# Kernel optimization log

Measured on AMD Instinct MI355X. Metric: run time of the kernel, lower is better.

## Reference

```python
import jax, jax.numpy as jnp
import numpy as np


def setup_inputs() -> dict:
    key = jax.random.key(0)
    ks = jax.random.split(key, 7)
    C, IC, H, W, B = 512, 256, 64, 64, 8
    N = H * W
    return {
        "x": jax.random.normal(ks[0], (B, C, H, W), dtype=jnp.float32),
        "w_phi": jax.random.normal(ks[1], (IC, C), dtype=jnp.float32) * 0.02,
        "w_theta": jax.random.normal(ks[2], (IC, C), dtype=jnp.float32) * 0.02,
        "w_g": jax.random.normal(ks[3], (IC, C), dtype=jnp.float32) * 0.02,
        "w_mask": jax.random.normal(ks[4], (C, IC), dtype=jnp.float32) * 0.02,
        "pos_embedding": jax.random.normal(ks[5], (1, N, N), dtype=jnp.float32),
        "pos_embedding_decoder": jax.random.normal(ks[6], (1, IC, H, W), dtype=jnp.float32),
    }


def reference(x, w_phi, w_theta, w_g, w_mask, pos_embedding, pos_embedding_decoder):
    b, c, h, w = x.shape
    n = h * w
    xf = x.reshape(b, c, n)  # [b, c, n]
    # 1x1 convs as channel matmuls
    phi = jnp.einsum('oc,bcn->bon', w_phi, xf)      # [b, ic, n]
    theta = jnp.einsum('oc,bcn->bon', w_theta, xf)  # [b, ic, n]
    g = jnp.einsum('oc,bcn->bon', w_g, xf) + pos_embedding_decoder.reshape(1, -1, n)
    g = jnp.swapaxes(g, 1, 2)  # [b, n, ic]
    # attention logits: theta^T @ phi -> [b, n_theta, n_phi], plus learned pos bias
    attn = jnp.einsum('bci,bcj->bij', theta, phi) + pos_embedding
    # NOTE: original softmax is over dim=1 (the theta/query axis), non-standard
    attn = jax.nn.softmax(attn, axis=1)
    y = jnp.einsum('bij,bjc->bic', attn, g)  # [b, n, ic]
    y = jnp.swapaxes(y, 1, 2).reshape(b, -1, n)  # [b, ic, n]
    mask = jnp.einsum('oc,bcn->bon', w_mask, y).reshape(b, c, h, w)
    return mask + x
```

## Files before the change

kernel.cpp:

```cpp
#include <hip/hip_runtime.h>

typedef short bf8 __attribute__((ext_vector_type(8)));
typedef float f32x4 __attribute__((ext_vector_type(4)));
typedef unsigned short us4 __attribute__((ext_vector_type(4)));
typedef unsigned short us8 __attribute__((ext_vector_type(8)));

#define DEVI __device__ __forceinline__

constexpr int NB = 8, NC = 512, NIC = 256, NS = 4096;

constexpr size_t OFF_XT  = 0;
constexpr size_t OFF_RS  = 0;
constexpr size_t OFF_TP  = 33554432;
constexpr size_t OFF_POS = 67108864;
constexpr size_t OFF_G   = 100663296;
constexpr size_t OFF_G2  = 117440512;
constexpr size_t OFF_Y   = 134217728;
constexpr size_t OFF_WTP = 150994944;
constexpr size_t OFF_WG  = 151519232;
constexpr size_t OFF_WM  = 151781376;

DEVI unsigned short f2bf(float f){
  unsigned u = __float_as_uint(f);
  u += 0x7fffu + ((u >> 16) & 1u);
  return (unsigned short)(u >> 16);
}
DEVI float bf2f(unsigned short b){ return __uint_as_float(((unsigned)b) << 16); }

DEVI void gld16(const void* g, void* l){
  __builtin_amdgcn_global_load_lds((const __attribute__((address_space(1))) unsigned int*)g,
                                   (__attribute__((address_space(3))) unsigned int*)l, 16, 0, 0);
}

DEVI void stageT(unsigned short* dst, const unsigned short* src, int ld, int wid, int lane){
  int rl = lane >> 3;
  int ce = ((lane & 7) << 3) ^ (rl << 3);
#pragma unroll
  for (int it = 0; it < 4; ++it){
    int q = wid + it * 4;
    gld16(src + (size_t)(q * 8 + rl) * ld + ce, dst + q * 512);
  }
}

DEVI void zero44(f32x4 (&a)[4][4]){
  f32x4 z = {0.f, 0.f, 0.f, 0.f};
#pragma unroll
  for (int i = 0; i < 4; ++i)
#pragma unroll
    for (int j = 0; j < 4; ++j) a[i][j] = z;
}

template<int NK64>
DEVI void gemm128v(const unsigned short* Ag, int lda, const unsigned short* Bg, int ldb,
                   unsigned short (&As)[2][8192], unsigned short (&Bs)[2][8192],
                   f32x4 (&acc)[4][4], int wid, int lane)
{
  const int wr = wid >> 1, wc = wid & 1;
  stageT(As[0], Ag, lda, wid, lane);
  stageT(Bs[0], Bg, ldb, wid, lane);
  __syncthreads();
  for (int kt = 0; kt < NK64; ++kt){
    int cur = kt & 1;
    if (kt + 1 < NK64){
      stageT(As[cur ^ 1], Ag + (kt + 1) * 64, lda, wid, lane);
      stageT(Bs[cur ^ 1], Bg + (kt + 1) * 64, ldb, wid, lane);
    }
    bf8 a[2][4], b[2][4];
#pragma unroll
    for (int ks = 0; ks < 2; ++ks){
      int cb = ks * 64 + ((lane >> 4) << 4);
#pragma unroll
      for (int f = 0; f < 4; ++f){
        int rA = wr * 64 + f * 16 + (lane & 15);
        a[ks][f] = *(const bf8*)((char*)As[cur] + rA * 128 + (cb ^ ((rA & 7) << 4)));
        int rB = wc * 64 + f * 16 + (lane & 15);
        b[ks][f] = *(const bf8*)((char*)Bs[cur] + rB * 128 + (cb ^ ((rB & 7) << 4)));
      }
    }
    __builtin_amdgcn_s_setprio(1);
#pragma unroll
    for (int ks = 0; ks < 2; ++ks)
#pragma unroll
      for (int i = 0; i < 4; ++i)
#pragma unroll
        for (int j = 0; j < 4; ++j)
          acc[i][j] = __builtin_amdgcn_mfma_f32_16x16x32_bf16(a[ks][i], b[ks][j], acc[i][j], 0, 0, 0);
    __builtin_amdgcn_s_setprio(0);
    __syncthreads();
  }
}


__global__ void k_prep(const float* wphi, const float* wtheta, const float* wgf, const float* wmf,
                       unsigned short* wtp, unsigned short* wgb, unsigned short* wmb){
  int idx = (blockIdx.x * 256 + threadIdx.x) * 4;
  const float* src; unsigned short* dst;
  if (idx < 131072)      { src = wphi + idx;            dst = wtp + idx; }
  else if (idx < 262144) { src = wtheta + (idx - 131072); dst = wtp + idx; }
  else if (idx < 393216) { src = wgf + (idx - 262144);  dst = wgb + (idx - 262144); }
  else                   { src = wmf + (idx - 393216);  dst = wmb + (idx - 393216); }
  f32x4 v = *(const f32x4*)src;
  us4 o;
#pragma unroll
  for (int r = 0; r < 4; ++r) o[r] = f2bf(v[r]);
  *(us4*)dst = o;
}

__global__ void k_pos(const float* pos, unsigned short* posb){
  size_t base = ((size_t)blockIdx.x * 256 + threadIdx.x) * 8;
  f32x4 v0 = *(const f32x4*)&pos[base];
  f32x4 v1 = *(const f32x4*)&pos[base + 4];
  us8 o;
#pragma unroll
  for (int r = 0; r < 4; ++r){ o[r] = f2bf(v0[r]); o[r + 4] = f2bf(v1[r]); }
  *(us8*)&posb[base] = o;
}

__global__ void k_xt(const float* x, unsigned short* xT){
  int b = blockIdx.z, ct = blockIdx.y, nt = blockIdx.x;
  __shared__ float t[64][65];
  int tid = threadIdx.x;
  int c0 = ct * 64, n0 = nt * 64;
  const float* xp = x + (size_t)b * NC * NS;
#pragma unroll
  for (int it = 0; it < 16; ++it){
    int idx = it * 256 + tid; int r = idx >> 6, cc = idx & 63;
    t[r][cc] = xp[(size_t)(c0 + r) * NS + n0 + cc];
  }
  __syncthreads();
  unsigned short* xo = xT + (size_t)b * NS * NC;
#pragma unroll
  for (int it = 0; it < 16; ++it){
    int idx = it * 256 + tid; int r = idx >> 6, cc = idx & 63;
    xo[(size_t)(n0 + r) * NC + c0 + cc] = f2bf(t[cc][r]);
  }
}


__global__ __launch_bounds__(256, 2) void k_tp(const unsigned short* wtp, const unsigned short* xT,
                                               unsigned short* tp){
  int b = blockIdx.z, ot = blockIdx.y, nt = blockIdx.x;
  int tid = threadIdx.x, wid = tid >> 6, lane = tid & 63, wr = wid >> 1, wc = wid & 1;
  __shared__ unsigned short As[2][8192], Bs[2][8192];
  f32x4 acc[4][4]; zero44(acc);
  gemm128v<8>(wtp + (size_t)(ot * 128) * 512, 512,
              xT + ((size_t)b * NS + nt * 128) * 512, 512, As, Bs, acc, wid, lane);
  unsigned short* out = tp + (size_t)b * NS * 512;
#pragma unroll
  for (int fr = 0; fr < 4; ++fr)
#pragma unroll
    for (int fc = 0; fc < 4; ++fc){
      int o0 = ot * 128 + wr * 64 + fr * 16 + ((lane >> 4) << 2);
      int n  = nt * 128 + wc * 64 + fc * 16 + (lane & 15);
      us4 v;
#pragma unroll
      for (int r = 0; r < 4; ++r) v[r] = f2bf(acc[fr][fc][r]);
      *(us4*)&out[(size_t)n * 512 + o0] = v;
    }
}

__global__ __launch_bounds__(256, 2) void k_g(const unsigned short* xT, const unsigned short* wgb,
                                              const float* pdec, unsigned short* gb){
  int b = blockIdx.z, ot = blockIdx.y, nt = blockIdx.x;
  int tid = threadIdx.x, wid = tid >> 6, lane = tid & 63, wr = wid >> 1, wc = wid & 1;
  __shared__ unsigned short As[2][8192], Bs[2][8192];
  f32x4 acc[4][4]; zero44(acc);
  gemm128v<8>(xT + ((size_t)b * NS + nt * 128) * 512, 512,
              wgb + (size_t)(ot * 128) * 512, 512, As, Bs, acc, wid, lane);
#pragma unroll
  for (int fr = 0; fr < 4; ++fr)
#pragma unroll
    for (int fc = 0; fc < 4; ++fc){
      int n0 = nt * 128 + wr * 64 + fr * 16 + ((lane >> 4) << 2);
      int o  = ot * 128 + wc * 64 + fc * 16 + (lane & 15);
      f32x4 pd = *(const f32x4*)&pdec[(size_t)o * NS + n0];
      us4 v;
#pragma unroll
      for (int r = 0; r < 4; ++r) v[r] = f2bf(acc[fr][fc][r] + pd[r]);
      *(us4*)&gb[((size_t)b * NIC + o) * NS + n0] = v;
    }
}

__global__ __launch_bounds__(256, 2) void k_stats(const unsigned short* __restrict__ tp,
                                                  const unsigned short* __restrict__ posb,
                                                  float* __restrict__ rs){
  int bid = blockIdx.x;
  int b = bid & 7, jb0 = (bid >> 3) * 64;
  int tid = threadIdx.x, wid = tid >> 6, lane = tid & 63;
  int p = wid >> 1, q = wid & 1, h = lane >> 4, l15 = lane & 15;
  __shared__ unsigned short Ath[4][8192];
  __shared__ float red[64];
  const unsigned short* tpb = tp + (size_t)b * NS * 512;

  bf8 bphi[8][2];
#pragma unroll
  for (int kb = 0; kb < 8; ++kb)
#pragma unroll
    for (int frj = 0; frj < 2; ++frj)
      bphi[kb][frj] = *(const bf8*)&tpb[(size_t)(jb0 + p * 32 + frj * 16 + l15) * 512
                                        + kb * 32 + h * 8];

  float sacc[2][4];
#pragma unroll
  for (int a = 0; a < 2; ++a)
#pragma unroll
    for (int r = 0; r < 4; ++r) sacc[a][r] = 0.f;

  stageT(Ath[0], tpb + 256, 512, wid, lane);
  stageT(Ath[1], tpb + 256 + 64, 512, wid, lane);

  for (int it = 0; it < 32; ++it){
    int i0t = it * 128;
    const unsigned short* thBase = tpb + (size_t)i0t * 512 + 256;
    const unsigned short* thNext = tpb + (size_t)(it < 31 ? i0t + 128 : i0t) * 512 + 256;
    us4 pv[2][4];
#pragma unroll
    for (int frj = 0; frj < 2; ++frj)
#pragma unroll
      for (int fci = 0; fci < 4; ++fci){
        int iG = i0t + q * 64 + fci * 16 + l15;
        int jG = jb0 + p * 32 + frj * 16 + h * 4;
        pv[frj][fci] = *(const us4*)&posb[(size_t)iG * NS + jG];
      }
    f32x4 lacc[2][4];
    {
      f32x4 z = {0.f, 0.f, 0.f, 0.f};
#pragma unroll
      for (int a = 0; a < 2; ++a)
#pragma unroll
        for (int c = 0; c < 4; ++c) lacc[a][c] = z;
    }
#pragma unroll
    for (int ph = 0; ph < 4; ++ph){
      const unsigned short* ssrc = (ph < 2) ? thBase + (ph + 2) * 64 : thNext + (ph - 2) * 64;
      stageT(Ath[(ph + 2) & 3], ssrc, 512, wid, lane);
      if (ph < 2) asm volatile("s_waitcnt vmcnt(16)" ::: "memory");
      else        asm volatile("s_waitcnt vmcnt(8)"  ::: "memory");
      __builtin_amdgcn_s_barrier();
      __builtin_amdgcn_sched_barrier(0);
#pragma unroll
      for (int ks = 0; ks < 2; ++ks){
        bf8 tfr[4];
#pragma unroll
        for (int fci = 0; fci < 4; ++fci){
          int rI = q * 64 + fci * 16 + l15;
          int cbyte = (ks * 64 + (h << 4)) ^ ((rI & 7) << 4);
          tfr[fci] = *(const bf8*)((char*)Ath[ph] + rI * 128 + cbyte);
        }
        __builtin_amdgcn_s_setprio(1);
#pragma unroll
        for (int frj = 0; frj < 2; ++frj)
#pragma unroll
          for (int fci = 0; fci < 4; ++fci)
            lacc[frj][fci] = __builtin_amdgcn_mfma_f32_16x16x32_bf16(bphi[ph * 2 + ks][frj], tfr[fci],
                                                                     lacc[frj][fci], 0, 0, 0);
        __builtin_amdgcn_s_setprio(0);
      }
    }
#pragma unroll
    for (int frj = 0; frj < 2; ++frj)
#pragma unroll
      for (int fci = 0; fci < 4; ++fci)
#pragma unroll
        for (int r = 0; r < 4; ++r)
          sacc[frj][r] += __expf(lacc[frj][fci][r] + bf2f(pv[frj][fci][r]));
  }
#pragma unroll
  for (int m = 1; m <= 8; m <<= 1)
#pragma unroll
    for (int frj = 0; frj < 2; ++frj)
#pragma unroll
      for (int r = 0; r < 4; ++r)
        sacc[frj][r] += __shfl_xor(sacc[frj][r], m, 64);
  if (q == 0 && l15 == 0){
#pragma unroll
    for (int frj = 0; frj < 2; ++frj)
#pragma unroll
      for (int r = 0; r < 4; ++r)
        red[p * 32 + frj * 16 + h * 4 + r] = sacc[frj][r];
  }
  __syncthreads();
  if (q == 1 && l15 == 0){
#pragma unroll
    for (int frj = 0; frj < 2; ++frj)
#pragma unroll
      for (int r = 0; r < 4; ++r){
        int jl = p * 32 + frj * 16 + h * 4 + r;
        float s = sacc[frj][r] + red[jl];
        rs[(size_t)b * NS + jb0 + jl] = 1.f / s;
      }
  }
}

__global__ void k_sg(const unsigned short* gb, const float* rs, unsigned short* g2){
  size_t base = ((size_t)blockIdx.x * 256 + threadIdx.x) * 8;
  int b = (int)(base / ((size_t)NIC * NS));
  int j0 = (int)(base % NS);
  const float* rsb = rs + (size_t)b * NS + j0;
  f32x4 r0 = *(const f32x4*)&rsb[0];
  f32x4 r1 = *(const f32x4*)&rsb[4];
  us8 gv = *(const us8*)&gb[base];
  us8 o;
#pragma unroll
  for (int r = 0; r < 4; ++r){
    o[r]     = f2bf(bf2f(gv[r])     * r0[r]);
    o[r + 4] = f2bf(bf2f(gv[r + 4]) * r1[r]);
  }
  *(us8*)&g2[base] = o;
}

__global__ __launch_bounds__(256, 2) void k_y(const unsigned short* __restrict__ tp,
                                              const unsigned short* __restrict__ posb,
                                              const unsigned short* __restrict__ g2,
                                              unsigned short* __restrict__ yb){
  int bid = blockIdx.x;
  int b = bid & 7, i0 = (bid >> 3) * 64;
  int tid = threadIdx.x, wid = tid >> 6, lane = tid & 63;
  int p = wid >> 1, q = wid & 1;
  __shared__ unsigned short Aph[4][8192];
  __shared__ unsigned short El[64 * 128];
  const unsigned short* tpb = tp + (size_t)b * NS * 512;

  bf8 btr[8][2];
#pragma unroll
  for (int kb = 0; kb < 8; ++kb)
#pragma unroll
    for (int fc = 0; fc < 2; ++fc)
      btr[kb][fc] = *(const bf8*)&tpb[(size_t)(i0 + p * 32 + fc * 16 + (lane & 15)) * 512
                                      + 256 + kb * 32 + (lane >> 4) * 8];

  f32x4 yacc[4][4]; zero44(yacc);
  stageT(Aph[0], tpb, 512, wid, lane);
  stageT(Aph[1], tpb + 64, 512, wid, lane);

  const unsigned short* g2b = g2 + (size_t)b * NIC * NS;

  for (int jt = 0; jt < 32; ++jt){
    int j0 = jt * 128;
    const unsigned short* phiBase = tpb + (size_t)j0 * 512;
    const unsigned short* phiNext = tpb + (size_t)(jt < 31 ? j0 + 128 : j0) * 512;
    us4 pv[4][2];
#pragma unroll
    for (int fr = 0; fr < 4; ++fr){
      int jl = q * 64 + fr * 16 + ((lane >> 4) << 2);
#pragma unroll
      for (int fc = 0; fc < 2; ++fc){
        int il = p * 32 + fc * 16 + (lane & 15);
        pv[fr][fc] = *(const us4*)&posb[(size_t)(i0 + il) * NS + j0 + jl];
      }
    }
    f32x4 lacc[4][2];
    {
      f32x4 z = {0.f, 0.f, 0.f, 0.f};
#pragma unroll
      for (int i = 0; i < 4; ++i)
#pragma unroll
        for (int j = 0; j < 2; ++j) lacc[i][j] = z;
    }
#pragma unroll
    for (int ph = 0; ph < 4; ++ph){
      const unsigned short* ssrc = (ph < 2) ? phiBase + (ph + 2) * 64 : phiNext + (ph - 2) * 64;
      stageT(Aph[(ph + 2) & 3], ssrc, 512, wid, lane);
      if (ph < 2) asm volatile("s_waitcnt vmcnt(16)" ::: "memory");
      else        asm volatile("s_waitcnt vmcnt(8)"  ::: "memory");
      __builtin_amdgcn_s_barrier();
      __builtin_amdgcn_sched_barrier(0);
#pragma unroll
      for (int ks = 0; ks < 2; ++ks){
        bf8 a[4];
#pragma unroll
        for (int fr = 0; fr < 4; ++fr){
          int r = q * 64 + fr * 16 + (lane & 15);
          int cbyte = (ks * 64 + ((lane >> 4) << 4)) ^ ((r & 7) << 4);
          a[fr] = *(const bf8*)((char*)Aph[ph] + r * 128 + cbyte);
        }
        __builtin_amdgcn_s_setprio(1);
#pragma unroll
        for (int fr = 0; fr < 4; ++fr)
#pragma unroll
          for (int fc = 0; fc < 2; ++fc)
            lacc[fr][fc] = __builtin_amdgcn_mfma_f32_16x16x32_bf16(a[fr], btr[ph * 2 + ks][fc],
                                                                   lacc[fr][fc], 0, 0, 0);
        __builtin_amdgcn_s_setprio(0);
      }
    }
#pragma unroll
    for (int fr = 0; fr < 4; ++fr)
#pragma unroll
      for (int fc = 0; fc < 2; ++fc){
        int il = p * 32 + fc * 16 + (lane & 15);
        int jl = q * 64 + fr * 16 + ((lane >> 4) << 2);
        us4 ev;
#pragma unroll
        for (int r = 0; r < 4; ++r)
          ev[r] = f2bf(__expf(lacc[fr][fc][r] + bf2f(pv[fr][fc][r])));
        *(us4*)((char*)El + il * 256 + ((jl * 2) ^ ((il & 7) << 4))) = ev;
      }
    __builtin_amdgcn_sched_barrier(0);
    asm volatile("s_waitcnt lgkmcnt(0)" ::: "memory");
    __builtin_amdgcn_s_barrier();
    __builtin_amdgcn_sched_barrier(0);
#pragma unroll
    for (int jk = 0; jk < 4; ++jk){
      bf8 eb[4];
#pragma unroll
      for (int f = 0; f < 4; ++f){
        int ei = f * 16 + (lane & 15);
        int ebt = jk * 64 + ((lane >> 4) << 4);
        eb[f] = *(const bf8*)((char*)El + ei * 256 + (ebt ^ ((ei & 7) << 4)));
      }
      __builtin_amdgcn_s_setprio(1);
#pragma unroll
      for (int cf = 0; cf < 4; ++cf){
        int c = wid * 64 + cf * 16 + (lane & 15);
        bf8 ga = *(const bf8*)&g2b[(size_t)c * NS + j0 + jk * 32 + (lane >> 4) * 8];
#pragma unroll
        for (int f = 0; f < 4; ++f)
          yacc[cf][f] = __builtin_amdgcn_mfma_f32_16x16x32_bf16(ga, eb[f], yacc[cf][f], 0, 0, 0);
      }
      __builtin_amdgcn_s_setprio(0);
    }
  }
  unsigned short* yo = yb + (size_t)b * NS * NIC;
#pragma unroll
  for (int cf = 0; cf < 4; ++cf)
#pragma unroll
    for (int f = 0; f < 4; ++f){
      int c0 = wid * 64 + cf * 16 + ((lane >> 4) << 2);
      int ig = i0 + f * 16 + (lane & 15);
      us4 v;
#pragma unroll
      for (int r = 0; r < 4; ++r) v[r] = f2bf(yacc[cf][f][r]);
      *(us4*)&yo[(size_t)ig * NIC + c0] = v;
    }
}

__global__ __launch_bounds__(256, 2) void k_out(const unsigned short* yb, const unsigned short* wmb,
                                                const float* xg, float* outg){
  int b = blockIdx.z, cot = blockIdx.y, nt = blockIdx.x;
  int tid = threadIdx.x, wid = tid >> 6, lane = tid & 63, wr = wid >> 1, wc = wid & 1;
  __shared__ unsigned short As[2][8192], Bs[2][8192];
  f32x4 acc[4][4]; zero44(acc);
  gemm128v<4>(yb + ((size_t)b * NS + nt * 128) * 256, 256,
              wmb + (size_t)(cot * 128) * 256, 256, As, Bs, acc, wid, lane);
#pragma unroll
  for (int fr = 0; fr < 4; ++fr)
#pragma unroll
    for (int fc = 0; fc < 4; ++fc){
      int n0 = nt * 128 + wr * 64 + fr * 16 + ((lane >> 4) << 2);
      int co = cot * 128 + wc * 64 + fc * 16 + (lane & 15);
      f32x4 xv = *(const f32x4*)&xg[((size_t)b * NC + co) * NS + n0];
      f32x4 ov = acc[fr][fc] + xv;
      *(f32x4*)&outg[((size_t)b * NC + co) * NS + n0] = ov;
    }
}

extern "C" void kernel_launch(void* const* d_in, const int* in_sizes, int n_in,
                              void* d_out, int out_size, void* d_ws, size_t ws_size,
                              hipStream_t stream){
  const float* x      = (const float*)d_in[0];
  const float* wphi   = (const float*)d_in[1];
  const float* wtheta = (const float*)d_in[2];
  const float* wgf    = (const float*)d_in[3];
  const float* wmf    = (const float*)d_in[4];
  const float* pos    = (const float*)d_in[5];
  const float* pdec   = (const float*)d_in[6];
  float* outg = (float*)d_out;
  char* ws = (char*)d_ws;
  unsigned short* xT   = (unsigned short*)(ws + OFF_XT);
  float*          rsv  = (float*)(ws + OFF_RS);
  unsigned short* tp   = (unsigned short*)(ws + OFF_TP);
  unsigned short* posb = (unsigned short*)(ws + OFF_POS);
  unsigned short* gb   = (unsigned short*)(ws + OFF_G);
  unsigned short* g2   = (unsigned short*)(ws + OFF_G2);
  unsigned short* yb   = (unsigned short*)(ws + OFF_Y);
  unsigned short* wtp  = (unsigned short*)(ws + OFF_WTP);
  unsigned short* wgb  = (unsigned short*)(ws + OFF_WG);
  unsigned short* wmb  = (unsigned short*)(ws + OFF_WM);

  k_prep<<<512, 256, 0, stream>>>(wphi, wtheta, wgf, wmf, wtp, wgb, wmb);
  k_pos<<<8192, 256, 0, stream>>>(pos, posb);
  k_xt<<<dim3(64, 8, 8), 256, 0, stream>>>(x, xT);
  k_tp<<<dim3(32, 4, 8), 256, 0, stream>>>(wtp, xT, tp);
  k_g<<<dim3(32, 2, 8), 256, 0, stream>>>(xT, wgb, pdec, gb);
  k_stats<<<512, 256, 0, stream>>>(tp, posb, rsv);
  k_sg<<<4096, 256, 0, stream>>>(gb, rsv, g2);
  k_y<<<512, 256, 0, stream>>>(tp, posb, g2, yb);
  k_out<<<dim3(32, 4, 8), 256, 0, stream>>>(yb, wmb, x, outg);
}
```

Measured before the change: 485.7 us.

## Split softmax column-sum kernel over query axis and reduce partials separately

The column-sum stats kernel now splits the 4096-row query loop into four chunks, launching 2048 blocks instead of 512 and writing partial sums that a new small kernel adds up and inverts. The LDS ring drops from four to three stages, with staging moved after the barrier, so occupancy can rise to three blocks per CU. The aim is to fill more of the GPU's CUs and hide latency better. The cost is an extra launch, a partial-sum buffer round trip, and phi fragments reloaded four times.

```diff
diff --git a/kernel.cpp b/kernel.cpp
--- a/kernel.cpp
+++ b/kernel.cpp
@@ -11,6 +11,7 @@
 
 constexpr size_t OFF_XT  = 0;
 constexpr size_t OFF_RS  = 0;
+constexpr size_t OFF_SP  = 262144;
 constexpr size_t OFF_TP  = 33554432;
 constexpr size_t OFF_POS = 67108864;
 constexpr size_t OFF_G   = 100663296;
@@ -181,14 +182,15 @@
     }
 }
 
-__global__ __launch_bounds__(256, 2) void k_stats(const unsigned short* __restrict__ tp,
-                                                  const unsigned short* __restrict__ posb,
-                                                  float* __restrict__ rs){
+__global__ __launch_bounds__(256, 3) void k_statsS(const unsigned short* __restrict__ tp,
+                                                   const unsigned short* __restrict__ posb,
+                                                   float* __restrict__ sp){
   int bid = blockIdx.x;
-  int b = bid & 7, jb0 = (bid >> 3) * 64;
+  int b = bid & 7, jblk = (bid >> 3) & 63, ih = bid >> 9;
+  int jb0 = jblk * 64;
   int tid = threadIdx.x, wid = tid >> 6, lane = tid & 63;
   int p = wid >> 1, q = wid & 1, h = lane >> 4, l15 = lane & 15;
-  __shared__ unsigned short Ath[4][8192];
+  __shared__ unsigned short Ath[3][8192];
   __shared__ float red[64];
   const unsigned short* tpb = tp + (size_t)b * NS * 512;
 
@@ -206,13 +208,16 @@
 #pragma unroll
     for (int r = 0; r < 4; ++r) sacc[a][r] = 0.f;
 
-  stageT(Ath[0], tpb + 256, 512, wid, lane);
-  stageT(Ath[1], tpb + 256 + 64, 512, wid, lane);
-
-  for (int it = 0; it < 32; ++it){
+  int it0 = ih * 8;
+  stageT(Ath[0], tpb + (size_t)(it0 * 128) * 512 + 256, 512, wid, lane);
+  stageT(Ath[1], tpb + (size_t)(it0 * 128) * 512 + 256 + 64, 512, wid, lane);
+
+  int sbase = 0;
+  for (int it = it0; it < it0 + 8; ++it){
     int i0t = it * 128;
     const unsigned short* thBase = tpb + (size_t)i0t * 512 + 256;
-    const unsigned short* thNext = tpb + (size_t)(it < 31 ? i0t + 128 : i0t) * 512 + 256;
+    int itn = (it < it0 + 7) ? it + 1 : it;
+    const unsigned short* thNext = tpb + (size_t)(itn * 128) * 512 + 256;
     us4 pv[2][4];
 #pragma unroll
     for (int frj = 0; frj < 2; ++frj)
@@ -232,12 +237,15 @@
     }
 #pragma unroll
     for (int ph = 0; ph < 4; ++ph){
-      const unsigned short* ssrc = (ph < 2) ? thBase + (ph + 2) * 64 : thNext + (ph - 2) * 64;
-      stageT(Ath[(ph + 2) & 3], ssrc, 512, wid, lane);
-      if (ph < 2) asm volatile("s_waitcnt vmcnt(16)" ::: "memory");
-      else        asm volatile("s_waitcnt vmcnt(8)"  ::: "memory");
+      if (ph < 2) asm volatile("s_waitcnt vmcnt(12)" ::: "memory");
+      else        asm volatile("s_waitcnt vmcnt(4)"  ::: "memory");
       __builtin_amdgcn_s_barrier();
       __builtin_amdgcn_sched_barrier(0);
+      const unsigned short* ssrc = (ph < 2) ? thBase + (ph + 2) * 64 : thNext + (ph - 2) * 64;
+      int sw = sbase + ph + 2; if (sw >= 3) sw -= 3; if (sw >= 3) sw -= 3;
+      stageT(Ath[sw], ssrc, 512, wid, lane);
+      __builtin_amdgcn_sched_barrier(0);
+      int sr = sbase + ph; if (sr >= 3) sr -= 3; if (sr >= 3) sr -= 3;
 #pragma unroll
       for (int ks = 0; ks < 2; ++ks){
         bf8 tfr[4];
@@ -245,7 +253,7 @@
         for (int fci = 0; fci < 4; ++fci){
           int rI = q * 64 + fci * 16 + l15;
           int cbyte = (ks * 64 + (h << 4)) ^ ((rI & 7) << 4);
-          tfr[fci] = *(const bf8*)((char*)Ath[ph] + rI * 128 + cbyte);
+          tfr[fci] = *(const bf8*)((char*)Ath[sr] + rI * 128 + cbyte);
         }
         __builtin_amdgcn_s_setprio(1);
 #pragma unroll
@@ -257,6 +265,7 @@
         __builtin_amdgcn_s_setprio(0);
       }
     }
+    sbase += 1; if (sbase >= 3) sbase = 0;
 #pragma unroll
     for (int frj = 0; frj < 2; ++frj)
 #pragma unroll
@@ -287,9 +296,17 @@
       for (int r = 0; r < 4; ++r){
         int jl = p * 32 + frj * 16 + h * 4 + r;
         float s = sacc[frj][r] + red[jl];
-        rs[(size_t)b * NS + jb0 + jl] = 1.f / s;
-      }
-  }
+        sp[(size_t)(ih * 8 + b) * NS + jb0 + jl] = s;
+      }
+  }
+}
+
+__global__ void k_rsF(const float* sp, float* rs){
+  int idx = blockIdx.x * 256 + threadIdx.x;
+  int b = idx >> 12, j = idx & 4095;
+  const float* s0 = sp + (size_t)b * NS + j;
+  float s = s0[0] + s0[(size_t)8 * NS] + s0[(size_t)16 * NS] + s0[(size_t)24 * NS];
+  rs[(size_t)b * NS + j] = 1.f / s;
 }
 
 __global__ void k_sg(const unsigned short* gb, const float* rs, unsigned short* g2){
@@ -469,6 +486,7 @@
   char* ws = (char*)d_ws;
   unsigned short* xT   = (unsigned short*)(ws + OFF_XT);
   float*          rsv  = (float*)(ws + OFF_RS);
+  float*          spv  = (float*)(ws + OFF_SP);
   unsigned short* tp   = (unsigned short*)(ws + OFF_TP);
   unsigned short* posb = (unsigned short*)(ws + OFF_POS);
   unsigned short* gb   = (unsigned short*)(ws + OFF_G);
@@ -483,7 +501,8 @@
   k_xt<<<dim3(64, 8, 8), 256, 0, stream>>>(x, xT);
   k_tp<<<dim3(32, 4, 8), 256, 0, stream>>>(wtp, xT, tp);
   k_g<<<dim3(32, 2, 8), 256, 0, stream>>>(xT, wgb, pdec, gb);
-  k_stats<<<512, 256, 0, stream>>>(tp, posb, rsv);
+  k_statsS<<<2048, 256, 0, stream>>>(tp, posb, spv);
+  k_rsF<<<128, 256, 0, stream>>>(spv, rsv);
   k_sg<<<4096, 256, 0, stream>>>(gb, rsv, g2);
   k_y<<<512, 256, 0, stream>>>(tp, posb, g2, yb);
   k_out<<<dim3(32, 4, 8), 256, 0, stream>>>(yb, wmb, x, outg);
```

Measured after the change: 505.2 us. 4.0% more time.
